# Optimization experiments

Hardware: AMD Instinct MI355X
Metric: run time of the kernel (lower is better)

## Reference

```python
import jax, jax.numpy as jnp
import numpy as np
import math

B, L, H, NH = 8, 200, 128, 2
HD = H // NH  # head dim = 64
TIME_VOCAB = 32
LN_EPS = 1e-12


def setup_inputs() -> dict:
    key = jax.random.key(0)
    ks = jax.random.split(key, 16)
    rn = lambda k, shape, s=0.02: (jax.random.normal(k, shape, jnp.float32) * s)
    return {
        "input_tensor": jax.random.normal(ks[0], (B, L, H), jnp.float32),
        "time_seq": jnp.sort(jax.random.randint(ks[1], (B, L), 0, 100000, jnp.int64), axis=-1),
        "attention_mask": jnp.zeros((B, 1, L, L), jnp.float32),
        "Wq": rn(ks[2], (H, H)), "bq": jnp.zeros((H,), jnp.float32),
        "Wk": rn(ks[3], (H, H)), "bk": jnp.zeros((H,), jnp.float32),
        "Wv": rn(ks[4], (H, H)), "bv": jnp.zeros((H,), jnp.float32),
        "Wd": rn(ks[5], (H, H)), "bd": jnp.zeros((H,), jnp.float32),
        "ln_g": jnp.ones((H,), jnp.float32), "ln_b": jnp.zeros((H,), jnp.float32),
        "key_time_table": rn(ks[6], (TIME_VOCAB, H)),
        "value_time_table": rn(ks[7], (TIME_VOCAB, H)),
        "key_pos_table": rn(ks[8], (L, H)),
        "value_pos_table": rn(ks[9], (L, H)),
    }


def _split_heads(x):
    # [B, L, H] -> [B, NH, L, HD]
    b, l, _ = x.shape
    return x.reshape(b, l, NH, HD).transpose(0, 2, 1, 3)


def reference(input_tensor, time_seq, attention_mask,
              Wq, bq, Wk, bk, Wv, bv, Wd, bd, ln_g, ln_b,
              key_time_table, value_time_table, key_pos_table, value_pos_table):
    b, l, h = input_tensor.shape

    # position embeddings (same for all batches)
    kpos = key_pos_table[:l].reshape(l, NH, HD).transpose(1, 0, 2)[None]    # [1,NH,L,HD]
    vpos = value_pos_table[:l].reshape(l, NH, HD).transpose(1, 0, 2)[None]  # [1,NH,L,HD]

    q = _split_heads(input_tensor @ Wq + bq)  # [B,NH,L,HD]
    k = _split_heads(input_tensor @ Wk + bk)
    v = _split_heads(input_tensor @ Wv + bv)

    scores = jnp.einsum('bhqd,bhkd->bhqk', q, k + kpos)

    # time decay: diff[b,i,j] = floor(log(1 + |t_i - t_j|))
    t = time_seq
    diff_idx = jnp.log1p(jnp.abs(t[:, :, None] - t[:, None, :]).astype(jnp.float32)).astype(jnp.int32)  # [B,L,L]

    # [B,L,L,H] -> [B,NH,L,L,HD]
    kt = key_time_table[diff_idx].reshape(b, l, l, NH, HD).transpose(0, 3, 1, 2, 4)
    vt = value_time_table[diff_idx].reshape(b, l, l, NH, HD).transpose(0, 3, 1, 2, 4)

    time_scores = jnp.einsum('bhqd,bhqkd->bhqk', q, kt)

    scores = (scores + time_scores) / math.sqrt(HD)
    scores = scores + attention_mask  # additive mask, broadcast over heads

    probs = jax.nn.softmax(scores, axis=-1)  # attn_dropout is identity in eval

    ctx = jnp.einsum('bhqk,bhkd->bhqd', probs, v + vpos)
    # NOTE: original uses raw (masked, pre-softmax) attention_scores here
    time_ctx = jnp.einsum('bhqk,bhqkd->bhqd', scores, vt)
    ctx = ctx + time_ctx

    ctx = ctx.transpose(0, 2, 1, 3).reshape(b, l, h)  # merge heads
    hidden = ctx @ Wd + bd                            # out_dropout identity in eval

    x = hidden + input_tensor
    mu = x.mean(-1, keepdims=True)
    var = ((x - mu) ** 2).mean(-1, keepdims=True)
    return (x - mu) / jnp.sqrt(var + LN_EPS) * ln_g + ln_b
```

## Files before the change

kernel.cpp:

```cpp
#include <hip/hip_runtime.h>
#include <math.h>

#define B_ 8
#define L_ 200
#define H_ 128
#define NH_ 2
#define HD_ 64
#define LP_ 256
#define TV_ 32
#define RQ_ 4

__global__ __launch_bounds__(128)
void qkv_kernel(const float* __restrict__ X,
                const float* __restrict__ Wq, const float* __restrict__ bq,
                const float* __restrict__ Wk, const float* __restrict__ bk,
                const float* __restrict__ Wv, const float* __restrict__ bv,
                const float* __restrict__ kpt, const float* __restrict__ vpt,
                float* __restrict__ Q, float* __restrict__ Kt, float* __restrict__ Vp){
    const int r0 = blockIdx.x * RQ_;
    const int m  = blockIdx.y;
    const int j  = threadIdx.x;
    __shared__ __align__(16) float xs[RQ_][H_];
    #pragma unroll
    for (int r = 0; r < RQ_; ++r) xs[r][j] = X[(r0 + r) * H_ + j];
    __syncthreads();
    const float* W = (m == 0) ? Wq : ((m == 1) ? Wk : Wv);
    float acc[RQ_];
    #pragma unroll
    for (int r = 0; r < RQ_; ++r) acc[r] = 0.f;
    #pragma unroll 4
    for (int i4 = 0; i4 < H_ / 4; ++i4) {
        const int i = i4 * 4;
        const float w0 = W[(i + 0) * H_ + j];
        const float w1 = W[(i + 1) * H_ + j];
        const float w2 = W[(i + 2) * H_ + j];
        const float w3 = W[(i + 3) * H_ + j];
        #pragma unroll
        for (int r = 0; r < RQ_; ++r) {
            const float4 xv = ((const float4*)xs[r])[i4];
            acc[r] += xv.x * w0 + xv.y * w1 + xv.z * w2 + xv.w * w3;
        }
    }
    const int h = j >> 6, d = j & 63;
    if (m == 0) {
        const float bj = bq[j];
        #pragma unroll
        for (int r = 0; r < RQ_; ++r) Q[(r0 + r) * H_ + j] = acc[r] + bj;
    } else if (m == 1) {
        const float bj = bk[j];
        #pragma unroll
        for (int r = 0; r < RQ_; ++r) {
            const int row = r0 + r, b = row / L_, l = row % L_;
            Kt[((b * NH_ + h) * HD_ + d) * LP_ + l] = acc[r] + bj + kpt[l * H_ + j];
        }
    } else {
        const float bj = bv[j];
        #pragma unroll
        for (int r = 0; r < RQ_; ++r) {
            const int row = r0 + r, b = row / L_, l = row % L_;
            Vp[((b * NH_ + h) * L_ + l) * HD_ + d] = acc[r] + bj + vpt[l * H_ + j];
        }
    }
}

__global__ __launch_bounds__(256)
void attn_out_kernel(const float* __restrict__ Q, const float* __restrict__ Kt,
                     const float* __restrict__ Vp, const int* __restrict__ tseq,
                     const float* __restrict__ mask,
                     const float* __restrict__ ktt, const float* __restrict__ vtt,
                     const float* __restrict__ Wd, const float* __restrict__ bd,
                     const float* __restrict__ X, const float* __restrict__ g,
                     const float* __restrict__ bb, float* __restrict__ out){
    const int b  = blockIdx.x / (L_ / 2);
    const int q0 = (blockIdx.x % (L_ / 2)) * 2;
    const int w  = threadIdx.x >> 6, lane = threadIdx.x & 63;
    const int h  = w & 1, qr = w >> 1;
    const int q  = q0 + qr;
    const int bh = b * NH_ + h;

    __shared__ __align__(16) float qs   [2][2][HD_];
    __shared__ float qkt_s[4][TV_];
    __shared__ float ss_s [4][TV_];
    __shared__ __align__(16) float ps_s [4][LP_];
    __shared__ __align__(16) float ctx_s[2][H_];
    __shared__ float redA[4], redB[4];

    qs[qr][h][lane] = Q[(b * L_ + q) * H_ + h * HD_ + lane];
    if (lane < TV_) ss_s[w][lane] = 0.f;

    {
        const int bkt = lane >> 1, half = lane & 1;
        const float4* kr4 = (const float4*)(ktt + bkt * H_ + h * HD_ + half * 32);
        const float4* qv4p = (const float4*)(&qs[qr][h][half * 32]);
        float a = 0.f;
        #pragma unroll
        for (int d4 = 0; d4 < 8; ++d4) {
            const float4 kv = kr4[d4];
            const float4 qv = qv4p[d4];
            a += qv.x * kv.x + qv.y * kv.y + qv.z * kv.z + qv.w * kv.w;
        }
        a += __shfl_xor(a, 1);
        if (half == 0) qkt_s[w][bkt] = a;
    }

    const float4* kt4 = (const float4*)(Kt + (size_t)bh * HD_ * LP_);
    const float4* qv4 = (const float4*)qs[qr][h];
    float4 s4 = make_float4(0.f, 0.f, 0.f, 0.f);
    #pragma unroll 4
    for (int d4 = 0; d4 < HD_ / 4; ++d4) {
        const float4 qq = qv4[d4];
        const float4 k0 = kt4[(d4 * 4 + 0) * (LP_ / 4) + lane];
        const float4 k1 = kt4[(d4 * 4 + 1) * (LP_ / 4) + lane];
        const float4 k2 = kt4[(d4 * 4 + 2) * (LP_ / 4) + lane];
        const float4 k3 = kt4[(d4 * 4 + 3) * (LP_ / 4) + lane];
        s4.x += qq.x * k0.x + qq.y * k1.x + qq.z * k2.x + qq.w * k3.x;
        s4.y += qq.x * k0.y + qq.y * k1.y + qq.z * k2.y + qq.w * k3.y;
        s4.z += qq.x * k0.z + qq.y * k1.z + qq.z * k2.z + qq.w * k3.z;
        s4.w += qq.x * k0.w + qq.y * k1.w + qq.z * k2.w + qq.w * k3.w;
    }
    float sv[4] = {s4.x, s4.y, s4.z, s4.w};
    const int k0i = lane * 4;
    float mx = -INFINITY;
    if (k0i < L_) {
        const float4 m4 = ((const float4*)(mask + ((size_t)(b * L_ + q)) * L_))[lane];
        const int4   t4 = ((const int4*)(tseq + b * L_))[lane];
        const int    tq = tseq[b * L_ + q];
        const float mv[4] = {m4.x, m4.y, m4.z, m4.w};
        const int   tk[4] = {t4.x, t4.y, t4.z, t4.w};
        #pragma unroll
        for (int jj = 0; jj < 4; ++jj) {
            int dt = tq - tk[jj]; if (dt < 0) dt = -dt;
            int ib = (int)log1pf((float)dt); if (ib > TV_ - 1) ib = TV_ - 1;
            const float s = (sv[jj] + qkt_s[w][ib]) * 0.125f + mv[jj];
            sv[jj] = s;
            atomicAdd(&ss_s[w][ib], s);
            if (s > mx) mx = s;
        }
    } else {
        sv[0] = sv[1] = sv[2] = sv[3] = -INFINITY;
    }
    #pragma unroll
    for (int off = 32; off; off >>= 1) { const float o = __shfl_xor(mx, off); if (o > mx) mx = o; }
    float sum = 0.f, ev[4];
    #pragma unroll
    for (int jj = 0; jj < 4; ++jj) {
        const float e = (k0i + jj < L_) ? __expf(sv[jj] - mx) : 0.f;
        ev[jj] = e; sum += e;
    }
    #pragma unroll
    for (int off = 32; off; off >>= 1) sum += __shfl_xor(sum, off);
    ((float4*)ps_s[w])[lane] = make_float4(ev[0], ev[1], ev[2], ev[3]);
    const float inv = 1.f / sum;

    {
        const int kk = lane >> 4, d4 = lane & 15;
        const float4* vp4 = (const float4*)(Vp + (size_t)bh * L_ * HD_);
        float4 c4 = make_float4(0.f, 0.f, 0.f, 0.f);
        #pragma unroll 5
        for (int kb = 0; kb < L_; kb += 4) {
            const float  p  = ps_s[w][kb + kk];
            const float4 vv = vp4[(kb + kk) * (HD_ / 4) + d4];
            c4.x += p * vv.x; c4.y += p * vv.y; c4.z += p * vv.z; c4.w += p * vv.w;
        }
        #pragma unroll
        for (int off = 16; off <= 32; off <<= 1) {
            c4.x += __shfl_xor(c4.x, off);
            c4.y += __shfl_xor(c4.y, off);
            c4.z += __shfl_xor(c4.z, off);
            c4.w += __shfl_xor(c4.w, off);
        }
        if (kk == 0) {
            c4.x *= inv; c4.y *= inv; c4.z *= inv; c4.w *= inv;
            *(float4*)&ctx_s[qr][h * HD_ + d4 * 4] = c4;
        }
    }
    {
        float tc = 0.f;
        #pragma unroll 8
        for (int i = 0; i < TV_; ++i) tc += ss_s[w][i] * vtt[i * H_ + h * HD_ + lane];
        ctx_s[qr][h * HD_ + lane] += tc;
    }
    __syncthreads();

    const int rr = threadIdx.x >> 7, j = threadIdx.x & 127;
    const float4* cr = (const float4*)ctx_s[rr];
    float acc = 0.f;
    #pragma unroll 8
    for (int i4 = 0; i4 < H_ / 4; ++i4) {
        const float4 xa = cr[i4];
        const int i = i4 * 4;
        acc += xa.x * Wd[(i + 0) * H_ + j];
        acc += xa.y * Wd[(i + 1) * H_ + j];
        acc += xa.z * Wd[(i + 2) * H_ + j];
        acc += xa.w * Wd[(i + 3) * H_ + j];
    }
    const int row = b * L_ + q0 + rr;
    const float x = acc + bd[j] + X[row * H_ + j];
    float s1 = x, s2 = x * x;
    #pragma unroll
    for (int off = 32; off; off >>= 1) { s1 += __shfl_xor(s1, off); s2 += __shfl_xor(s2, off); }
    if (lane == 0) { redA[w] = s1; redB[w] = s2; }
    __syncthreads();
    const float mean = (redA[2 * rr] + redA[2 * rr + 1]) * (1.f / H_);
    const float ex2  = (redB[2 * rr] + redB[2 * rr + 1]) * (1.f / H_);
    const float var  = ex2 - mean * mean;
    out[row * H_ + j] = (x - mean) * rsqrtf(var + 1e-12f) * g[j] + bb[j];
}

extern "C" void kernel_launch(void* const* d_in, const int* in_sizes, int n_in,
                              void* d_out, int out_size, void* d_ws, size_t ws_size,
                              hipStream_t stream) {
    const float* X    = (const float*)d_in[0];
    const int*   tseq = (const int*)  d_in[1];
    const float* mask = (const float*)d_in[2];
    const float* Wq = (const float*)d_in[3],  *bq = (const float*)d_in[4];
    const float* Wk = (const float*)d_in[5],  *bk = (const float*)d_in[6];
    const float* Wv = (const float*)d_in[7],  *bv = (const float*)d_in[8];
    const float* Wd = (const float*)d_in[9],  *bd = (const float*)d_in[10];
    const float* g  = (const float*)d_in[11], *bb = (const float*)d_in[12];
    const float* ktt = (const float*)d_in[13], *vtt = (const float*)d_in[14];
    const float* kpt = (const float*)d_in[15], *vpt = (const float*)d_in[16];

    float* ws  = (float*)d_ws;
    float* Q   = ws;
    float* Kt  = Q   + B_ * L_ * H_;
    float* Vp  = Kt  + B_ * NH_ * HD_ * LP_;

    dim3 g1(B_ * L_ / RQ_, 3);
    qkv_kernel<<<g1, 128, 0, stream>>>(X, Wq, bq, Wk, bk, Wv, bv, kpt, vpt, Q, Kt, Vp);
    attn_out_kernel<<<B_ * (L_ / 2), 256, 0, stream>>>(Q, Kt, Vp, tseq, mask, ktt, vtt,
                                                       Wd, bd, X, g, bb, (float*)d_out);
}
```

Before: 122.0 us.

## Fuse QKV projection into attention kernel with per-batch spin-wait flags

Merges the separate QKV projection kernel into the attention/output kernel. Each block projects its own two rows into Q (kept in shared memory), K and V, publishes a release flag, then spin-waits until all blocks of the same batch have written K/V. This removes one kernel launch and the global round trip for Q, and reuses the staged X for the residual. It adds a memset launch and relies on all 800 blocks being co-resident (launch_bounds 256,4), which risks deadlock or stalls from spinning.

```diff
diff --git a/kernel.cpp b/kernel.cpp
--- a/kernel.cpp
+++ b/kernel.cpp
@@ -8,89 +8,75 @@
 #define HD_ 64
 #define LP_ 256
 #define TV_ 32
-#define RQ_ 4
-
-__global__ __launch_bounds__(128)
-void qkv_kernel(const float* __restrict__ X,
-                const float* __restrict__ Wq, const float* __restrict__ bq,
-                const float* __restrict__ Wk, const float* __restrict__ bk,
-                const float* __restrict__ Wv, const float* __restrict__ bv,
-                const float* __restrict__ kpt, const float* __restrict__ vpt,
-                float* __restrict__ Q, float* __restrict__ Kt, float* __restrict__ Vp){
-    const int r0 = blockIdx.x * RQ_;
-    const int m  = blockIdx.y;
-    const int j  = threadIdx.x;
-    __shared__ __align__(16) float xs[RQ_][H_];
-    #pragma unroll
-    for (int r = 0; r < RQ_; ++r) xs[r][j] = X[(r0 + r) * H_ + j];
-    __syncthreads();
-    const float* W = (m == 0) ? Wq : ((m == 1) ? Wk : Wv);
-    float acc[RQ_];
-    #pragma unroll
-    for (int r = 0; r < RQ_; ++r) acc[r] = 0.f;
-    #pragma unroll 4
-    for (int i4 = 0; i4 < H_ / 4; ++i4) {
-        const int i = i4 * 4;
-        const float w0 = W[(i + 0) * H_ + j];
-        const float w1 = W[(i + 1) * H_ + j];
-        const float w2 = W[(i + 2) * H_ + j];
-        const float w3 = W[(i + 3) * H_ + j];
-        #pragma unroll
-        for (int r = 0; r < RQ_; ++r) {
-            const float4 xv = ((const float4*)xs[r])[i4];
-            acc[r] += xv.x * w0 + xv.y * w1 + xv.z * w2 + xv.w * w3;
-        }
-    }
-    const int h = j >> 6, d = j & 63;
-    if (m == 0) {
-        const float bj = bq[j];
-        #pragma unroll
-        for (int r = 0; r < RQ_; ++r) Q[(r0 + r) * H_ + j] = acc[r] + bj;
-    } else if (m == 1) {
-        const float bj = bk[j];
-        #pragma unroll
-        for (int r = 0; r < RQ_; ++r) {
-            const int row = r0 + r, b = row / L_, l = row % L_;
-            Kt[((b * NH_ + h) * HD_ + d) * LP_ + l] = acc[r] + bj + kpt[l * H_ + j];
-        }
-    } else {
-        const float bj = bv[j];
-        #pragma unroll
-        for (int r = 0; r < RQ_; ++r) {
-            const int row = r0 + r, b = row / L_, l = row % L_;
-            Vp[((b * NH_ + h) * L_ + l) * HD_ + d] = acc[r] + bj + vpt[l * H_ + j];
-        }
-    }
-}
-
-__global__ __launch_bounds__(256)
-void attn_out_kernel(const float* __restrict__ Q, const float* __restrict__ Kt,
-                     const float* __restrict__ Vp, const int* __restrict__ tseq,
-                     const float* __restrict__ mask,
-                     const float* __restrict__ ktt, const float* __restrict__ vtt,
-                     const float* __restrict__ Wd, const float* __restrict__ bd,
-                     const float* __restrict__ X, const float* __restrict__ g,
-                     const float* __restrict__ bb, float* __restrict__ out){
+#define NBLK_ (B_ * (L_ / 2))
+
+__global__ __launch_bounds__(256, 4)
+void fused_kernel(const float* __restrict__ X,
+                  const float* __restrict__ Wq, const float* __restrict__ bq,
+                  const float* __restrict__ Wk, const float* __restrict__ bk,
+                  const float* __restrict__ Wv, const float* __restrict__ bv,
+                  const float* __restrict__ kpt, const float* __restrict__ vpt,
+                  const int*   __restrict__ tseq, const float* __restrict__ mask,
+                  const float* __restrict__ ktt, const float* __restrict__ vtt,
+                  const float* __restrict__ Wd,  const float* __restrict__ bd,
+                  const float* __restrict__ g,   const float* __restrict__ bb,
+                  float* Kt, float* Vp, unsigned* flags, float* __restrict__ out){
     const int b  = blockIdx.x / (L_ / 2);
     const int q0 = (blockIdx.x % (L_ / 2)) * 2;
-    const int w  = threadIdx.x >> 6, lane = threadIdx.x & 63;
-    const int h  = w & 1, qr = w >> 1;
-    const int q  = q0 + qr;
-    const int bh = b * NH_ + h;
 
     __shared__ __align__(16) float qs   [2][2][HD_];
+    __shared__ __align__(16) float xs   [2][H_];
     __shared__ float qkt_s[4][TV_];
     __shared__ float ss_s [4][TV_];
     __shared__ __align__(16) float ps_s [4][LP_];
     __shared__ __align__(16) float ctx_s[2][H_];
     __shared__ float redA[4], redB[4];
 
-    qs[qr][h][lane] = Q[(b * L_ + q) * H_ + h * HD_ + lane];
+    {
+        const int j = threadIdx.x, r = j >> 7, c = j & 127;
+        xs[r][c] = X[(b * L_ + q0 + r) * H_ + c];
+        __syncthreads();
+        float aq = 0.f, ak = 0.f, av = 0.f;
+        const float4* xv4 = (const float4*)xs[r];
+        #pragma unroll 2
+        for (int i4 = 0; i4 < H_ / 4; ++i4) {
+            const float4 xv = xv4[i4];
+            const int i = i4 * 4;
+            aq += xv.x * Wq[(i + 0) * H_ + c] + xv.y * Wq[(i + 1) * H_ + c]
+                + xv.z * Wq[(i + 2) * H_ + c] + xv.w * Wq[(i + 3) * H_ + c];
+            ak += xv.x * Wk[(i + 0) * H_ + c] + xv.y * Wk[(i + 1) * H_ + c]
+                + xv.z * Wk[(i + 2) * H_ + c] + xv.w * Wk[(i + 3) * H_ + c];
+            av += xv.x * Wv[(i + 0) * H_ + c] + xv.y * Wv[(i + 1) * H_ + c]
+                + xv.z * Wv[(i + 2) * H_ + c] + xv.w * Wv[(i + 3) * H_ + c];
+        }
+        const int h = c >> 6, d = c & 63, l = q0 + r;
+        qs[r][h][d] = aq + bq[c];
+        Kt[((b * NH_ + h) * HD_ + d) * LP_ + l] = ak + bk[c] + kpt[l * H_ + c];
+        Vp[((b * NH_ + h) * L_ + l) * HD_ + d]  = av + bv[c] + vpt[l * H_ + c];
+    }
+    __syncthreads();
+    if (threadIdx.x == 0)
+        __hip_atomic_store(&flags[blockIdx.x], 1u, __ATOMIC_RELEASE, __HIP_MEMORY_SCOPE_AGENT);
+    {
+        const int base = b * (L_ / 2);
+        for (int i = threadIdx.x; i < L_ / 2; i += 256)
+            while (__hip_atomic_load(&flags[base + i], __ATOMIC_ACQUIRE,
+                                     __HIP_MEMORY_SCOPE_AGENT) == 0u)
+                __builtin_amdgcn_s_sleep(2);
+    }
+    __syncthreads();
+    __threadfence();
+
+    const int w = threadIdx.x >> 6, lane = threadIdx.x & 63;
+    const int h = w & 1, qr = w >> 1;
+    const int q = q0 + qr;
+    const int bh = b * NH_ + h;
+
     if (lane < TV_) ss_s[w][lane] = 0.f;
 
     {
         const int bkt = lane >> 1, half = lane & 1;
-        const float4* kr4 = (const float4*)(ktt + bkt * H_ + h * HD_ + half * 32);
+        const float4* kr4  = (const float4*)(ktt + bkt * H_ + h * HD_ + half * 32);
         const float4* qv4p = (const float4*)(&qs[qr][h][half * 32]);
         float a = 0.f;
         #pragma unroll
@@ -195,7 +181,7 @@
         acc += xa.w * Wd[(i + 3) * H_ + j];
     }
     const int row = b * L_ + q0 + rr;
-    const float x = acc + bd[j] + X[row * H_ + j];
+    const float x = acc + bd[j] + xs[rr][j];
     float s1 = x, s2 = x * x;
     #pragma unroll
     for (int off = 32; off; off >>= 1) { s1 += __shfl_xor(s1, off); s2 += __shfl_xor(s2, off); }
@@ -221,13 +207,14 @@
     const float* ktt = (const float*)d_in[13], *vtt = (const float*)d_in[14];
     const float* kpt = (const float*)d_in[15], *vpt = (const float*)d_in[16];
 
-    float* ws  = (float*)d_ws;
-    float* Q   = ws;
-    float* Kt  = Q   + B_ * L_ * H_;
-    float* Vp  = Kt  + B_ * NH_ * HD_ * LP_;
-
-    dim3 g1(B_ * L_ / RQ_, 3);
-    qkv_kernel<<<g1, 128, 0, stream>>>(X, Wq, bq, Wk, bk, Wv, bv, kpt, vpt, Q, Kt, Vp);
-    attn_out_kernel<<<B_ * (L_ / 2), 256, 0, stream>>>(Q, Kt, Vp, tseq, mask, ktt, vtt,
-                                                       Wd, bd, X, g, bb, (float*)d_out);
+    float*    ws    = (float*)d_ws;
+    float*    Kt    = ws;
+    float*    Vp    = Kt + B_ * NH_ * HD_ * LP_;
+    unsigned* flags = (unsigned*)(Vp + B_ * L_ * H_);
+
+    hipMemsetAsync(flags, 0, NBLK_ * sizeof(unsigned), stream);
+
+    fused_kernel<<<NBLK_, 256, 0, stream>>>(X, Wq, bq, Wk, bk, Wv, bv, kpt, vpt,
+                                            tseq, mask, ktt, vtt, Wd, bd, g, bb,
+                                            Kt, Vp, flags, (float*)d_out);
 }
```

Measured after the change: 285.2 us. 2.34x slower.
